# Kernel optimization log

Hardware: AMD Instinct MI355X
Metric: run time of the kernel (lower is better)

The kernel has to match this reference:

```python
import jax, jax.numpy as jnp
import numpy as np
import math

B, S, H, DM = 1, 2048, 16, 1024
DK = DM // H
MAX_SEQ = 2048  # rel_embed has MAX_SEQ+1 rows


def setup_inputs() -> dict:
    rng = jax.random.key(0)
    ks = jax.random.split(rng, 12)
    w = lambda k, shape, s=0.02: (jax.random.normal(k, shape, jnp.float32) * s)
    inp = {
        'query': jax.random.normal(ks[0], (B, S, DM), jnp.float32),
        'key':   jax.random.normal(ks[1], (B, S, DM), jnp.float32),
        'value': jax.random.normal(ks[2], (B, S, DM), jnp.float32),
        # causal integer mask [B,S,S] (cumsum over it derives rel-pos indices)
        'mask': jnp.broadcast_to(jnp.tril(jnp.ones((S, S), jnp.int32)), (B, S, S)),
        'Wq': w(ks[3], (DM, DM)), 'bq': jnp.zeros((DM,), jnp.float32),
        'Wk': w(ks[4], (DM, DM)), 'bk': jnp.zeros((DM,), jnp.float32),
        'Wv': w(ks[5], (DM, DM)), 'bv': jnp.zeros((DM,), jnp.float32),
        'Wo': w(ks[6], (DM, DM)), 'bo': jnp.zeros((DM,), jnp.float32),
        # relative position embeddings [h, max_seq_len+1, d_k], N(0,1) as in the module
        'rel_embed': jax.random.normal(ks[7], (H, MAX_SEQ + 1, DK), jnp.float32),
    }
    return inp


def reference(query, key, value, mask, Wq, bq, Wk, bk, Wv, bv, Wo, bo, rel_embed):
    scale = 1.0 / math.sqrt(DK)
    heads = lambda x, W, b: (x @ W.T + b).reshape(B, S, H, DK).transpose(0, 2, 1, 3)
    q = heads(query, Wq, bq)   # [B,H,S,DK]
    k = heads(key, Wk, bk)
    v = heads(value, Wv, bv)

    scores = jnp.einsum('bhid,bhjd->bhij', q, k) * scale  # [B,H,S,S]

    m4 = mask[:, None, :, :]                 # [B,1,S,S]
    nz = m4 != 0
    # torch: cumsum(mask)-1 picks the m-index; index 0 (then zeroed) where mask==0
    m_idx = jnp.where(nz, jnp.cumsum(m4, axis=-1) - 1, 0)  # [B,1,S,S]

    # rel_scores[b,h,m,l] = <q[b,h,l,:], rel_embed[h,m,:]> / sqrt(d_k)
    rel = jnp.einsum('bhld,hmd->bhml', q, rel_embed[:, :S]) * scale  # [B,H,S,S]
    idx = jnp.broadcast_to(m_idx, (B, H, S, S))
    # torch.take flat-index decodes to rel[b,h, m_idx[i,j], j]
    rel_g = jnp.take_along_axis(rel, idx, axis=2) * nz.astype(scores.dtype)

    scores = jnp.where(nz, scores + rel_g, jnp.float32(-1e9))
    p = jax.nn.softmax(scores, axis=-1)      # dropout p=0.0 -> identity

    out = jnp.einsum('bhij,bhjd->bhid', p, v)         # [B,H,S,DK]
    out = out.transpose(0, 2, 1, 3).reshape(B, S, DM)  # [B,S,DM]
    return out @ Wo.T + bo
```

## Files before the change

### kernel.cpp

```cpp
#include <hip/hip_runtime.h>

typedef __bf16 bf16_t;
typedef __bf16 bf16x4 __attribute__((ext_vector_type(4)));
typedef __bf16 bf16x8 __attribute__((ext_vector_type(8)));
typedef float  f32x4  __attribute__((ext_vector_type(4)));
typedef float  f32x16 __attribute__((ext_vector_type(16)));
typedef unsigned int u32;

#define S_LEN 2048
#define DMODEL 1024
#define NHEAD 16
#define DHEAD 64
#define RELROWS 2049

__device__ __forceinline__ void gload16(const void* g, void* l) {
    __builtin_amdgcn_global_load_lds((const __attribute__((address_space(1))) void*)g,
                                     (__attribute__((address_space(3))) void*)l,
                                     16, 0, 0);
}

__device__ __forceinline__ f32x4 mfma16(bf16x8 a, bf16x8 b, f32x4 c) {
    return __builtin_amdgcn_mfma_f32_16x16x32_bf16(a, b, c, 0, 0, 0);
}
__device__ __forceinline__ f32x16 mfma32(bf16x8 a, bf16x8 b, f32x16 c) {
    return __builtin_amdgcn_mfma_f32_32x32x16_bf16(a, b, c, 0, 0, 0);
}

__device__ __forceinline__ bf16x8 lds_read_swz(const bf16_t* base, int row, int colb) {
    return *(const bf16x8*)((const char*)base + row * 128 + (colb ^ ((row & 7) << 4)));
}

__device__ __forceinline__ u32 cvtpk(float lo, float hi) {
    u32 w;
    asm("v_cvt_pk_bf16_f32 %0, %1, %2" : "=v"(w) : "v"(lo), "v"(hi));
    return w;
}
__device__ __forceinline__ void swap32(u32& a, u32& b) {
    asm("v_permlane32_swap_b32 %0, %1" : "+v"(a), "+v"(b));
}

__global__ __launch_bounds__(256)
void f2bf4(const float* __restrict__ s0, const float* __restrict__ s1,
           const float* __restrict__ s2, const float* __restrict__ s3,
           bf16_t* __restrict__ dst, int n4) {
    const int z = blockIdx.y;
    const float* src = (z == 0) ? s0 : (z == 1) ? s1 : (z == 2) ? s2 : s3;
    int i = blockIdx.x * blockDim.x + threadIdx.x;
    if (i >= n4) return;
    float4 v = ((const float4*)src)[i];
    bf16x4 o;
    o[0] = (bf16_t)v.x; o[1] = (bf16_t)v.y; o[2] = (bf16_t)v.z; o[3] = (bf16_t)v.w;
    ((bf16x4*)(dst + (size_t)z * n4 * 4))[i] = o;
}

template <int MODE, int BM, int BN>
__global__ __launch_bounds__(256)
void gemm_bt(const bf16_t* __restrict__ Abase, const bf16_t* __restrict__ Wbase,
             const float* __restrict__ b0, const float* __restrict__ b1,
             const float* __restrict__ b2,
             bf16_t* __restrict__ outb, float* __restrict__ outf,
             int M, int N, int K) {
    __shared__ alignas(16) bf16_t As[BM * 64];
    __shared__ alignas(16) bf16_t Bs[BN * 64];
    const int tid = threadIdx.x, lane = tid & 63, wave = tid >> 6;
    const int z = blockIdx.z;
    const bf16_t* A = Abase + (size_t)z * M * K;
    const bf16_t* W = Wbase + (size_t)z * N * K;
    const float* bias = (z == 0) ? b0 : (z == 1 ? b1 : b2);
    const int nwg = gridDim.x * gridDim.y;
    const int wg = blockIdx.y * gridDim.x + blockIdx.x;
    const int swz = (wg & 7) * (nwg >> 3) + (wg >> 3);
    const int m0 = (swz / gridDim.x) * BM, n0 = (swz % gridDim.x) * BN;
    const int wr = (wave >> 1) * (BM / 2), wc = (wave & 1) * (BN / 2);
    constexpr int MR = BM / 32, NR = BN / 32;

    f32x4 acc[MR][NR] = {};
    const int soff = wave * 1024 + lane * 16;

    for (int kt = 0; kt < K; kt += 64) {
#pragma unroll
        for (int r = 0; r < BM / 32; ++r) {
            int e = (r * 4096 + soff) >> 1;
            int row = e >> 6, col = e & 63;
            gload16(A + (size_t)(m0 + row) * K + kt + col, (char*)As + r * 4096 + wave * 1024);
        }
#pragma unroll
        for (int r = 0; r < BN / 32; ++r) {
            int e = (r * 4096 + soff) >> 1;
            int row = e >> 6, col = e & 63;
            gload16(W + (size_t)(n0 + row) * K + kt + col, (char*)Bs + r * 4096 + wave * 1024);
        }
        __syncthreads();
#pragma unroll
        for (int kk = 0; kk < 2; ++kk) {
            bf16x8 af[MR], bfr[NR];
#pragma unroll
            for (int m = 0; m < MR; ++m)
                af[m] = *(const bf16x8*)&As[(wr + m * 16 + (lane & 15)) * 64 + kk * 32 + (lane >> 4) * 8];
#pragma unroll
            for (int n = 0; n < NR; ++n)
                bfr[n] = *(const bf16x8*)&Bs[(wc + n * 16 + (lane & 15)) * 64 + kk * 32 + (lane >> 4) * 8];
#pragma unroll
            for (int m = 0; m < MR; ++m)
#pragma unroll
                for (int n = 0; n < NR; ++n)
                    acc[m][n] = mfma16(af[m], bfr[n], acc[m][n]);
        }
        __syncthreads();
    }

    const float scale = (MODE == 0 && z == 0) ? 0.125f : 1.0f;
#pragma unroll
    for (int m = 0; m < MR; ++m) {
        const int gi = m0 + wr + m * 16 + (lane >> 4) * 4;
#pragma unroll
        for (int n = 0; n < NR; ++n) {
            const int gj = n0 + wc + n * 16 + (lane & 15);
            const float bv = bias[gj];
#pragma unroll
            for (int r2 = 0; r2 < 4; ++r2) {
                float v = (acc[m][n][r2] + bv) * scale;
                if (MODE == 0)
                    outb[(size_t)z * M * N + (size_t)(gi + r2) * N + gj] = (bf16_t)v;
                else
                    outf[(size_t)(gi + r2) * N + gj] = v;
            }
        }
    }
}

__global__ __launch_bounds__(256)
void prep_v(const bf16_t* __restrict__ Qb, const float* __restrict__ rel,
            const bf16_t* __restrict__ V,
            bf16_t* __restrict__ Vtp, bf16_t* __restrict__ ErG) {
    __shared__ float t[64][65];
    __shared__ float ers[64];
    const int s0 = blockIdx.x * 64, h = blockIdx.y;
    const int tid = threadIdx.x;
    {
        const int j = tid >> 2, dq = tid & 3;
        const bf16_t* qp = Qb + (size_t)(s0 + j) * DMODEL + h * DHEAD + dq * 16;
        const float* rp = rel + ((size_t)h * RELROWS + (s0 + j)) * DHEAD + dq * 16;
        bf16x8 q0 = *(const bf16x8*)qp;
        bf16x8 q1 = *(const bf16x8*)(qp + 8);
        float4 r0 = *(const float4*)(rp + 0), r1 = *(const float4*)(rp + 4);
        float4 r2 = *(const float4*)(rp + 8), r3 = *(const float4*)(rp + 12);
        float acc = 0.f;
        acc += (float)q0[0] * r0.x + (float)q0[1] * r0.y + (float)q0[2] * r0.z + (float)q0[3] * r0.w;
        acc += (float)q0[4] * r1.x + (float)q0[5] * r1.y + (float)q0[6] * r1.z + (float)q0[7] * r1.w;
        acc += (float)q1[0] * r2.x + (float)q1[1] * r2.y + (float)q1[2] * r2.z + (float)q1[3] * r2.w;
        acc += (float)q1[4] * r3.x + (float)q1[5] * r3.y + (float)q1[6] * r3.z + (float)q1[7] * r3.w;
        acc += __shfl_xor(acc, 1);
        acc += __shfl_xor(acc, 2);
        if (dq == 0) {
            float er = __expf(acc);
            ers[j] = er;
            ErG[h * S_LEN + s0 + j] = (bf16_t)er;
        }
    }
    __syncthreads();
#pragma unroll
    for (int it = 0; it < 16; ++it) {
        int idx = it * 256 + tid;
        int r = idx >> 6, c = idx & 63;
        t[r][c] = (float)V[(size_t)(s0 + r) * DMODEL + h * DHEAD + c] * ers[r];
    }
    __syncthreads();
#pragma unroll
    for (int it = 0; it < 16; ++it) {
        int idx = it * 256 + tid;
        int r = idx >> 6, c = idx & 63;
        Vtp[(size_t)(h * DHEAD + r) * S_LEN + s0 + c] = (bf16_t)t[c][r];
    }
}

__global__ __launch_bounds__(256, 2)
void flash_attn(const bf16_t* __restrict__ Qb, const bf16_t* __restrict__ Kb,
                const bf16_t* __restrict__ Vtp, const bf16_t* __restrict__ ErG,
                bf16_t* __restrict__ Ob) {
    __shared__ alignas(16) bf16_t KB[4][64 * 64];
    __shared__ alignas(16) bf16_t VB[4][64 * 64];
    __shared__ alignas(16) bf16_t Qs[64 * 64];
    __shared__ bf16_t Ers[S_LEN];
    const int tid = threadIdx.x, lane = tid & 63, wave = tid >> 6;
    const int qt = (int)gridDim.x - 1 - (int)blockIdx.x;
    const int h = blockIdx.y;
    const int q0 = qt * 64;
    const int nt = qt + 1;
    const int lo5 = lane & 31, hi = lane >> 5;
    const int qhalf = wave & 1;
    const int par = wave >> 1;

    const int nkv = nt * 64;
    if (tid * 8 < nkv)
        *(bf16x8*)&Ers[tid * 8] = *(const bf16x8*)&ErG[h * S_LEN + tid * 8];

    auto stage_tile = [&](int tt) {
        const int bse = tt & 3;
#pragma unroll
        for (int r2 = 0; r2 < 2; ++r2) {
            int rr = wave * 2 + r2;
            int L = rr * 1024 + lane * 16;
            int row = L >> 7, colb = (L & 127) ^ ((row & 7) << 4);
            gload16(Kb + (size_t)(tt * 64 + row) * DMODEL + h * DHEAD + (colb >> 1),
                    (char*)KB[bse] + rr * 1024);
            gload16(Vtp + (size_t)(h * DHEAD + row) * S_LEN + tt * 64 + (colb >> 1),
                    (char*)VB[bse] + rr * 1024);
        }
    };

#pragma unroll
    for (int r2 = 0; r2 < 2; ++r2) {
        int rr = wave * 2 + r2;
        int L = rr * 1024 + lane * 16;
        int row = L >> 7, colb = (L & 127) ^ ((row & 7) << 4);
        gload16(Qb + (size_t)(q0 + row) * DMODEL + h * DHEAD + (colb >> 1),
                (char*)Qs + rr * 1024);
    }
    stage_tile(0);
    stage_tile(nt > 1 ? 1 : 0);
    asm volatile("s_waitcnt vmcnt(8) lgkmcnt(0)\n\ts_barrier" ::: "memory");

    bf16x8 qf[4];
#pragma unroll
    for (int c = 0; c < 4; ++c)
        qf[c] = lds_read_swz(Qs, qhalf * 32 + lo5, c * 32 + hi * 16);

    f32x16 oacc[2] = {};
    float ls = 0.f;

    for (int t2 = 0; t2 < nt; t2 += 2) {
        if (t2 + 3 < nt) {
            stage_tile(t2 + 2);
            stage_tile(t2 + 3);
            asm volatile("s_waitcnt vmcnt(8)\n\ts_barrier" ::: "memory");
        } else if (t2 + 2 < nt) {
            stage_tile(t2 + 2);
            asm volatile("s_waitcnt vmcnt(4)\n\ts_barrier" ::: "memory");
        } else {
            asm volatile("s_waitcnt vmcnt(0)\n\ts_barrier" ::: "memory");
        }

        const int tt = t2 + par;
        if (tt < nt) {
            const int buf = tt & 3;
            const int kv0 = tt * 64;
            const bool diag = (tt == nt - 1);
            u32 pw[4][4];
#pragma unroll
            for (int kb = 0; kb < 2; ++kb) {
                f32x16 st = {};
#pragma unroll
                for (int c = 0; c < 4; ++c) {
                    bf16x8 kf = lds_read_swz(KB[buf], kb * 32 + lo5, c * 32 + hi * 16);
                    st = mfma32(kf, qf[c], st);
                }
                bf16x4 erv[4];
#pragma unroll
                for (int g = 0; g < 4; ++g)
                    erv[g] = *(const bf16x4*)&Ers[kv0 + kb * 32 + g * 8 + hi * 4];
                float pr[16];
                if (diag) {
#pragma unroll
                    for (int r = 0; r < 16; ++r) {
                        int kloc = kb * 32 + (r & 3) + 8 * (r >> 2) + 4 * hi;
                        float v = __expf(st[r]);
                        pr[r] = (kloc > qhalf * 32 + lo5) ? 0.f : v;
                    }
                } else {
#pragma unroll
                    for (int r = 0; r < 16; ++r) pr[r] = __expf(st[r]);
                }
#pragma unroll
                for (int r = 0; r < 16; ++r)
                    ls += pr[r] * (float)erv[r >> 2][r & 3];
#pragma unroll
                for (int hf = 0; hf < 2; ++hf) {
                    u32 a  = cvtpk(pr[8 * hf + 0], pr[8 * hf + 1]);
                    u32 b  = cvtpk(pr[8 * hf + 4], pr[8 * hf + 5]);
                    swap32(a, b);
                    u32 c2 = cvtpk(pr[8 * hf + 2], pr[8 * hf + 3]);
                    u32 d2 = cvtpk(pr[8 * hf + 6], pr[8 * hf + 7]);
                    swap32(c2, d2);
                    pw[kb * 2 + hf][0] = a;  pw[kb * 2 + hf][1] = c2;
                    pw[kb * 2 + hf][2] = b;  pw[kb * 2 + hf][3] = d2;
                }
            }
#pragma unroll
            for (int kc = 0; kc < 4; ++kc) {
                union { u32 w[4]; bf16x8 v; } uu;
                uu.w[0] = pw[kc][0]; uu.w[1] = pw[kc][1]; uu.w[2] = pw[kc][2]; uu.w[3] = pw[kc][3];
#pragma unroll
                for (int db = 0; db < 2; ++db) {
                    bf16x8 vf = lds_read_swz(VB[buf], db * 32 + lo5, kc * 32 + hi * 16);
                    oacc[db] = mfma32(vf, uu.v, oacc[db]);
                }
            }
        }
        asm volatile("s_barrier" ::: "memory");
    }

    asm volatile("s_waitcnt vmcnt(0)" ::: "memory");
    if (wave >= 2) {
        char* base = (char*)KB[0] + (wave - 2) * 9728 + lane * 144;
#pragma unroll
        for (int db = 0; db < 2; ++db)
#pragma unroll
            for (int g = 0; g < 4; ++g) {
                f32x4 v4;
#pragma unroll
                for (int e = 0; e < 4; ++e) v4[e] = oacc[db][g * 4 + e];
                *(f32x4*)(base + (db * 4 + g) * 16) = v4;
            }
        *(float*)((char*)KB[0] + 19456 + (wave - 2) * 256 + lane * 4) = ls;
    }
    __syncthreads();
    if (wave < 2) {
        const char* base = (const char*)KB[0] + wave * 9728 + lane * 144;
#pragma unroll
        for (int db = 0; db < 2; ++db)
#pragma unroll
            for (int g = 0; g < 4; ++g) {
                f32x4 v4 = *(const f32x4*)(base + (db * 4 + g) * 16);
#pragma unroll
                for (int e = 0; e < 4; ++e) oacc[db][g * 4 + e] += v4[e];
            }
        ls += *(const float*)((const char*)KB[0] + 19456 + wave * 256 + lane * 4);
        ls += __shfl_xor(ls, 32);
        const float inv = 1.0f / ls;
        const int qg = q0 + wave * 32 + lo5;
#pragma unroll
        for (int db = 0; db < 2; ++db)
#pragma unroll
            for (int g = 0; g < 4; ++g) {
                bf16x4 o4;
#pragma unroll
                for (int e = 0; e < 4; ++e)
                    o4[e] = (bf16_t)(oacc[db][g * 4 + e] * inv);
                *(bf16x4*)&Ob[(size_t)qg * DMODEL + h * DHEAD + db * 32 + g * 8 + hi * 4] = o4;
            }
    }
}

extern "C" void kernel_launch(void* const* d_in, const int* in_sizes, int n_in,
                              void* d_out, int out_size, void* d_ws, size_t ws_size,
                              hipStream_t stream) {
    const float* query = (const float*)d_in[0];
    const float* key   = (const float*)d_in[1];
    const float* value = (const float*)d_in[2];
    const float* Wq  = (const float*)d_in[4];
    const float* bq  = (const float*)d_in[5];
    const float* Wk  = (const float*)d_in[6];
    const float* bk  = (const float*)d_in[7];
    const float* Wv  = (const float*)d_in[8];
    const float* bv  = (const float*)d_in[9];
    const float* Wo  = (const float*)d_in[10];
    const float* bo  = (const float*)d_in[11];
    const float* rel = (const float*)d_in[12];

    char* ws = (char*)d_ws;
    const size_t nX = (size_t)S_LEN * DMODEL;
    const size_t nW = (size_t)DMODEL * DMODEL;
    bf16_t* Xbf  = (bf16_t*)ws;
    bf16_t* Wbf  = (bf16_t*)(ws + 3 * nX * 2);
    bf16_t* QKV  = (bf16_t*)(ws + 3 * nX * 2 + 4 * nW * 2);
    bf16_t* Vtp  = (bf16_t*)ws;
    bf16_t* AOb  = (bf16_t*)(ws + nX * 2);
    bf16_t* ErG  = (bf16_t*)(ws + 2 * nX * 2);
    (void)in_sizes; (void)n_in; (void)out_size; (void)ws_size;

    const int n4X = (int)(nX / 4), n4W = (int)(nW / 4);
    f2bf4<<<dim3(n4X / 256, 3), 256, 0, stream>>>(query, key, value, nullptr, Xbf, n4X);
    f2bf4<<<dim3(n4W / 256, 4), 256, 0, stream>>>(Wq, Wk, Wv, Wo, Wbf, n4W);

    gemm_bt<0, 128, 64><<<dim3(DMODEL / 64, S_LEN / 128, 3), 256, 0, stream>>>(
        Xbf, Wbf, bq, bk, bv, QKV, nullptr, S_LEN, DMODEL, DMODEL);

    prep_v<<<dim3(S_LEN / 64, NHEAD), 256, 0, stream>>>(QKV, rel, QKV + 2 * nX, Vtp, ErG);
    flash_attn<<<dim3(S_LEN / 64, NHEAD), 256, 0, stream>>>(QKV, QKV + nX, Vtp, ErG, AOb);

    gemm_bt<1, 64, 64><<<dim3(DMODEL / 64, S_LEN / 64, 1), 256, 0, stream>>>(
        AOb, Wbf + 3 * nW, bo, bo, bo, nullptr, (float*)d_out, S_LEN, DMODEL, DMODEL);
}
```

Baseline: 95.56 us.

## Double-buffer GEMM loads, fold rel bias into score accumulator, merge conversions

The projection GEMM now double-buffers its LDS tiles and issues the next K-tile's global loads before computing the current one, waiting with explicit vmcnt counts instead of full barriers. The relative-position bias is kept as fp32 logits and used as the initial value of the QK^T accumulator, so the per-column exp multiply on V and on the row sum goes away. This also removes the bf16 rounding of exp(rel). The two fp32-to-bf16 conversion launches become a single launch, and s_setprio hints are placed around the MFMA sections. The costs are twice the GEMM LDS, a larger fp32 rel buffer in flash_attn shared memory, and hand-coded vmcnt values that must match the number of loads issued per stage.

```diff
diff --git a/kernel.cpp b/kernel.cpp
--- a/kernel.cpp
+++ b/kernel.cpp
@@ -40,17 +40,28 @@
 }
 
 __global__ __launch_bounds__(256)
-void f2bf4(const float* __restrict__ s0, const float* __restrict__ s1,
-           const float* __restrict__ s2, const float* __restrict__ s3,
-           bf16_t* __restrict__ dst, int n4) {
-    const int z = blockIdx.y;
-    const float* src = (z == 0) ? s0 : (z == 1) ? s1 : (z == 2) ? s2 : s3;
-    int i = blockIdx.x * blockDim.x + threadIdx.x;
-    if (i >= n4) return;
-    float4 v = ((const float4*)src)[i];
+void f2bf_all(const float* __restrict__ xq, const float* __restrict__ xk,
+              const float* __restrict__ xv,
+              const float* __restrict__ wq, const float* __restrict__ wk,
+              const float* __restrict__ wv, const float* __restrict__ wo,
+              bf16_t* __restrict__ dst, int n4X, int n4W) {
+    const int i = blockIdx.x * blockDim.x + threadIdx.x;
+    const float* src; int j;
+    if (i < 3 * n4X) {
+        if (i < n4X)            { src = xq; j = i; }
+        else if (i < 2 * n4X)   { src = xk; j = i - n4X; }
+        else                    { src = xv; j = i - 2 * n4X; }
+    } else {
+        int w = i - 3 * n4X;
+        if (w < n4W)            { src = wq; j = w; }
+        else if (w < 2 * n4W)   { src = wk; j = w - n4W; }
+        else if (w < 3 * n4W)   { src = wv; j = w - 2 * n4W; }
+        else                    { src = wo; j = w - 3 * n4W; }
+    }
+    float4 v = ((const float4*)src)[j];
     bf16x4 o;
     o[0] = (bf16_t)v.x; o[1] = (bf16_t)v.y; o[2] = (bf16_t)v.z; o[3] = (bf16_t)v.w;
-    ((bf16x4*)(dst + (size_t)z * n4 * 4))[i] = o;
+    ((bf16x4*)dst)[i] = o;
 }
 
 template <int MODE, int BM, int BN>
@@ -60,8 +71,8 @@
              const float* __restrict__ b2,
              bf16_t* __restrict__ outb, float* __restrict__ outf,
              int M, int N, int K) {
-    __shared__ alignas(16) bf16_t As[BM * 64];
-    __shared__ alignas(16) bf16_t Bs[BN * 64];
+    __shared__ alignas(16) bf16_t As[2][BM * 64];
+    __shared__ alignas(16) bf16_t Bs[2][BN * 64];
     const int tid = threadIdx.x, lane = tid & 63, wave = tid >> 6;
     const int z = blockIdx.z;
     const bf16_t* A = Abase + (size_t)z * M * K;
@@ -73,40 +84,57 @@
     const int m0 = (swz / gridDim.x) * BM, n0 = (swz % gridDim.x) * BN;
     const int wr = (wave >> 1) * (BM / 2), wc = (wave & 1) * (BN / 2);
     constexpr int MR = BM / 32, NR = BN / 32;
+    constexpr int LOADS = BM / 32 + BN / 32;
 
     f32x4 acc[MR][NR] = {};
     const int soff = wave * 1024 + lane * 16;
 
-    for (int kt = 0; kt < K; kt += 64) {
+    auto stage = [&](int b, int kt) {
 #pragma unroll
         for (int r = 0; r < BM / 32; ++r) {
             int e = (r * 4096 + soff) >> 1;
             int row = e >> 6, col = e & 63;
-            gload16(A + (size_t)(m0 + row) * K + kt + col, (char*)As + r * 4096 + wave * 1024);
+            gload16(A + (size_t)(m0 + row) * K + kt + col,
+                    (char*)As[b] + r * 4096 + wave * 1024);
         }
 #pragma unroll
         for (int r = 0; r < BN / 32; ++r) {
             int e = (r * 4096 + soff) >> 1;
             int row = e >> 6, col = e & 63;
-            gload16(W + (size_t)(n0 + row) * K + kt + col, (char*)Bs + r * 4096 + wave * 1024);
-        }
-        __syncthreads();
+            gload16(W + (size_t)(n0 + row) * K + kt + col,
+                    (char*)Bs[b] + r * 4096 + wave * 1024);
+        }
+    };
+
+    const int NK = K >> 6;
+    stage(0, 0);
+    for (int s = 0; s < NK; ++s) {
+        const int buf = s & 1;
+        if (s + 1 < NK) {
+            stage(buf ^ 1, (s + 1) << 6);
+            if constexpr (LOADS == 6) asm volatile("s_waitcnt vmcnt(6)" ::: "memory");
+            else if constexpr (LOADS == 4) asm volatile("s_waitcnt vmcnt(4)" ::: "memory");
+            else asm volatile("s_waitcnt vmcnt(8)" ::: "memory");
+        } else {
+            asm volatile("s_waitcnt vmcnt(0)" ::: "memory");
+        }
+        asm volatile("s_barrier" ::: "memory");
 #pragma unroll
         for (int kk = 0; kk < 2; ++kk) {
             bf16x8 af[MR], bfr[NR];
 #pragma unroll
             for (int m = 0; m < MR; ++m)
-                af[m] = *(const bf16x8*)&As[(wr + m * 16 + (lane & 15)) * 64 + kk * 32 + (lane >> 4) * 8];
+                af[m] = *(const bf16x8*)&As[buf][(wr + m * 16 + (lane & 15)) * 64 + kk * 32 + (lane >> 4) * 8];
 #pragma unroll
             for (int n = 0; n < NR; ++n)
-                bfr[n] = *(const bf16x8*)&Bs[(wc + n * 16 + (lane & 15)) * 64 + kk * 32 + (lane >> 4) * 8];
+                bfr[n] = *(const bf16x8*)&Bs[buf][(wc + n * 16 + (lane & 15)) * 64 + kk * 32 + (lane >> 4) * 8];
 #pragma unroll
             for (int m = 0; m < MR; ++m)
 #pragma unroll
                 for (int n = 0; n < NR; ++n)
                     acc[m][n] = mfma16(af[m], bfr[n], acc[m][n]);
         }
-        __syncthreads();
+        asm volatile("s_barrier" ::: "memory");
     }
 
     const float scale = (MODE == 0 && z == 0) ? 0.125f : 1.0f;
@@ -132,9 +160,8 @@
 __global__ __launch_bounds__(256)
 void prep_v(const bf16_t* __restrict__ Qb, const float* __restrict__ rel,
             const bf16_t* __restrict__ V,
-            bf16_t* __restrict__ Vtp, bf16_t* __restrict__ ErG) {
+            bf16_t* __restrict__ Vtp, float* __restrict__ RG) {
     __shared__ float t[64][65];
-    __shared__ float ers[64];
     const int s0 = blockIdx.x * 64, h = blockIdx.y;
     const int tid = threadIdx.x;
     {
@@ -152,18 +179,13 @@
         acc += (float)q1[4] * r3.x + (float)q1[5] * r3.y + (float)q1[6] * r3.z + (float)q1[7] * r3.w;
         acc += __shfl_xor(acc, 1);
         acc += __shfl_xor(acc, 2);
-        if (dq == 0) {
-            float er = __expf(acc);
-            ers[j] = er;
-            ErG[h * S_LEN + s0 + j] = (bf16_t)er;
-        }
-    }
-    __syncthreads();
+        if (dq == 0) RG[h * S_LEN + s0 + j] = acc;
+    }
 #pragma unroll
     for (int it = 0; it < 16; ++it) {
         int idx = it * 256 + tid;
         int r = idx >> 6, c = idx & 63;
-        t[r][c] = (float)V[(size_t)(s0 + r) * DMODEL + h * DHEAD + c] * ers[r];
+        t[r][c] = (float)V[(size_t)(s0 + r) * DMODEL + h * DHEAD + c];
     }
     __syncthreads();
 #pragma unroll
@@ -176,12 +198,12 @@
 
 __global__ __launch_bounds__(256, 2)
 void flash_attn(const bf16_t* __restrict__ Qb, const bf16_t* __restrict__ Kb,
-                const bf16_t* __restrict__ Vtp, const bf16_t* __restrict__ ErG,
+                const bf16_t* __restrict__ Vtp, const float* __restrict__ RG,
                 bf16_t* __restrict__ Ob) {
     __shared__ alignas(16) bf16_t KB[4][64 * 64];
     __shared__ alignas(16) bf16_t VB[4][64 * 64];
     __shared__ alignas(16) bf16_t Qs[64 * 64];
-    __shared__ bf16_t Ers[S_LEN];
+    __shared__ alignas(16) float Rs[S_LEN];
     const int tid = threadIdx.x, lane = tid & 63, wave = tid >> 6;
     const int qt = (int)gridDim.x - 1 - (int)blockIdx.x;
     const int h = blockIdx.y;
@@ -192,8 +214,12 @@
     const int par = wave >> 1;
 
     const int nkv = nt * 64;
-    if (tid * 8 < nkv)
-        *(bf16x8*)&Ers[tid * 8] = *(const bf16x8*)&ErG[h * S_LEN + tid * 8];
+    if (tid * 8 < nkv) {
+        float4 a = *(const float4*)&RG[h * S_LEN + tid * 8];
+        float4 b = *(const float4*)&RG[h * S_LEN + tid * 8 + 4];
+        *(float4*)&Rs[tid * 8] = a;
+        *(float4*)&Rs[tid * 8 + 4] = b;
+    }
 
     auto stage_tile = [&](int tt) {
         const int bse = tt & 3;
@@ -249,16 +275,20 @@
             u32 pw[4][4];
 #pragma unroll
             for (int kb = 0; kb < 2; ++kb) {
-                f32x16 st = {};
+                f32x16 st;
+#pragma unroll
+                for (int g = 0; g < 4; ++g) {
+                    f32x4 rv = *(const f32x4*)&Rs[kv0 + kb * 32 + g * 8 + hi * 4];
+#pragma unroll
+                    for (int e = 0; e < 4; ++e) st[g * 4 + e] = rv[e];
+                }
+                __builtin_amdgcn_s_setprio(1);
 #pragma unroll
                 for (int c = 0; c < 4; ++c) {
                     bf16x8 kf = lds_read_swz(KB[buf], kb * 32 + lo5, c * 32 + hi * 16);
                     st = mfma32(kf, qf[c], st);
                 }
-                bf16x4 erv[4];
-#pragma unroll
-                for (int g = 0; g < 4; ++g)
-                    erv[g] = *(const bf16x4*)&Ers[kv0 + kb * 32 + g * 8 + hi * 4];
+                __builtin_amdgcn_s_setprio(0);
                 float pr[16];
                 if (diag) {
 #pragma unroll
@@ -272,8 +302,7 @@
                     for (int r = 0; r < 16; ++r) pr[r] = __expf(st[r]);
                 }
 #pragma unroll
-                for (int r = 0; r < 16; ++r)
-                    ls += pr[r] * (float)erv[r >> 2][r & 3];
+                for (int r = 0; r < 16; ++r) ls += pr[r];
 #pragma unroll
                 for (int hf = 0; hf < 2; ++hf) {
                     u32 a  = cvtpk(pr[8 * hf + 0], pr[8 * hf + 1]);
@@ -286,6 +315,7 @@
                     pw[kb * 2 + hf][2] = b;  pw[kb * 2 + hf][3] = d2;
                 }
             }
+            __builtin_amdgcn_s_setprio(1);
 #pragma unroll
             for (int kc = 0; kc < 4; ++kc) {
                 union { u32 w[4]; bf16x8 v; } uu;
@@ -296,6 +326,7 @@
                     oacc[db] = mfma32(vf, uu.v, oacc[db]);
                 }
             }
+            __builtin_amdgcn_s_setprio(0);
         }
         asm volatile("s_barrier" ::: "memory");
     }
@@ -366,18 +397,19 @@
     bf16_t* QKV  = (bf16_t*)(ws + 3 * nX * 2 + 4 * nW * 2);
     bf16_t* Vtp  = (bf16_t*)ws;
     bf16_t* AOb  = (bf16_t*)(ws + nX * 2);
-    bf16_t* ErG  = (bf16_t*)(ws + 2 * nX * 2);
+    float*  RG   = (float*)(ws + 2 * nX * 2);
     (void)in_sizes; (void)n_in; (void)out_size; (void)ws_size;
 
     const int n4X = (int)(nX / 4), n4W = (int)(nW / 4);
-    f2bf4<<<dim3(n4X / 256, 3), 256, 0, stream>>>(query, key, value, nullptr, Xbf, n4X);
-    f2bf4<<<dim3(n4W / 256, 4), 256, 0, stream>>>(Wq, Wk, Wv, Wo, Wbf, n4W);
+    const int tot4 = 3 * n4X + 4 * n4W;
+    f2bf_all<<<tot4 / 256, 256, 0, stream>>>(query, key, value, Wq, Wk, Wv, Wo,
+                                             Xbf, n4X, n4W);
 
     gemm_bt<0, 128, 64><<<dim3(DMODEL / 64, S_LEN / 128, 3), 256, 0, stream>>>(
         Xbf, Wbf, bq, bk, bv, QKV, nullptr, S_LEN, DMODEL, DMODEL);
 
-    prep_v<<<dim3(S_LEN / 64, NHEAD), 256, 0, stream>>>(QKV, rel, QKV + 2 * nX, Vtp, ErG);
-    flash_attn<<<dim3(S_LEN / 64, NHEAD), 256, 0, stream>>>(QKV, QKV + nX, Vtp, ErG, AOb);
+    prep_v<<<dim3(S_LEN / 64, NHEAD), 256, 0, stream>>>(QKV, rel, QKV + 2 * nX, Vtp, RG);
+    flash_attn<<<dim3(S_LEN / 64, NHEAD), 256, 0, stream>>>(QKV, QKV + nX, Vtp, RG, AOb);
 
     gemm_bt<1, 64, 64><<<dim3(DMODEL / 64, S_LEN / 64, 1), 256, 0, stream>>>(
         AOb, Wbf + 3 * nW, bo, bo, bo, nullptr, (float*)d_out, S_LEN, DMODEL, DMODEL);
```

Result: faster. 89.63 us (-6.2%).
